# Optimization experiments

Hardware: AMD Instinct MI355X
Metric: run time of the kernel (lower is better)

Reference implementation:

```python
import jax, jax.numpy as jnp
import numpy as np

DIM = 768
HEADS = 12
HIDDEN = 3072  # int(dim * mlp_ratio)
DEGREE = 3
EPS = 1e-5


def layer_norm(x, g, b):
    m = jnp.mean(x, axis=-1, keepdims=True)
    v = jnp.mean((x - m) ** 2, axis=-1, keepdims=True)
    return (x - m) * jax.lax.rsqrt(v + EPS) * g + b


def cheby_layer(x, coeffs):
    # x: (B, N, I); coeffs: (I, O, DEGREE+1)
    t = jnp.tanh(x)
    theta = jnp.arccos(t)  # (B, N, I)
    d = jnp.arange(DEGREE + 1, dtype=x.dtype)
    basis = jnp.cos(theta[..., None] * d)  # (B, N, I, D)
    return jnp.einsum('bnid,iod->bno', basis, coeffs)


def setup_inputs() -> dict:
    key = jax.random.key(0)
    ks = jax.random.split(key, 9)
    B, N, C, H = 32, 197, DIM, HIDDEN
    x = jax.random.normal(ks[0], (B, N, C), dtype=jnp.float32)
    g1 = jnp.ones((C,), jnp.float32)
    b1 = jnp.zeros((C,), jnp.float32)
    w_qkv = jax.random.normal(ks[1], (C, 3 * C), jnp.float32) * (C ** -0.5)
    w_proj = jax.random.normal(ks[2], (C, C), jnp.float32) * (C ** -0.5)
    b_proj = jnp.zeros((C,), jnp.float32)
    g2 = jnp.ones((C,), jnp.float32)
    b2 = jnp.zeros((C,), jnp.float32)
    c1 = jax.random.normal(ks[3], (C, H, DEGREE + 1), jnp.float32) / (C * (DEGREE + 1))
    c2 = jax.random.normal(ks[4], (H, C, DEGREE + 1), jnp.float32) / (H * (DEGREE + 1))
    return {"x": x, "g1": g1, "b1": b1, "w_qkv": w_qkv, "w_proj": w_proj,
            "b_proj": b_proj, "g2": g2, "b2": b2, "c1": c1, "c2": c2}


def reference(x, g1, b1, w_qkv, w_proj, b_proj, g2, b2, c1, c2):
    B, N, C = x.shape
    hd = C // HEADS
    scale = hd ** -0.5
    # --- attention branch ---
    h = layer_norm(x, g1, b1)
    qkv = (h @ w_qkv).reshape(B, N, 3, HEADS, hd).transpose(2, 0, 3, 1, 4)
    q, k, v = qkv[0], qkv[1], qkv[2]  # (B, H, N, hd)
    attn = jax.nn.softmax(jnp.einsum('bhnd,bhmd->bhnm', q, k) * scale, axis=-1)
    o = jnp.einsum('bhnm,bhmd->bhnd', attn, v).transpose(0, 2, 1, 3).reshape(B, N, C)
    x = x + o @ w_proj + b_proj
    # --- ChebyKAN MLP branch ---
    h = layer_norm(x, g2, b2)
    h = cheby_layer(h, c1)   # (B, N, HIDDEN)
    h = cheby_layer(h, c2)   # (B, N, C)
    return x + h
```

## Files before the change

### kernel.cpp

```cpp
#include <hip/hip_runtime.h>
#include <hip/hip_bf16.h>
#include <cmath>
#include <cstdint>
#include <cstddef>

#define DEV __device__ __forceinline__

typedef __attribute__((ext_vector_type(4))) float f32x4;
typedef __attribute__((ext_vector_type(8))) short bf16x8;
typedef __attribute__((ext_vector_type(4))) unsigned int u32x4;
typedef __attribute__((ext_vector_type(4))) unsigned short u16x4;

constexpr int NBATCH = 32;
constexpr int SEQ    = 197;
constexpr int CH     = 768;
constexpr int H3     = 3 * CH;
constexpr int NHEADS = 12;
constexpr int HD     = 64;
constexpr int HID    = 3072;
constexpr int TOK    = NBATCH * SEQ;
constexpr int TOKP   = 6400;
constexpr int KSPLIT = 2;
constexpr float LNEPS = 1e-5f;

DEV unsigned short f2bf(float f) {
  unsigned int u = __builtin_bit_cast(unsigned int, f);
  u += 0x7fffu + ((u >> 16) & 1u);
  return (unsigned short)(u >> 16);
}
DEV float bf2f(unsigned short s) {
  unsigned int u = ((unsigned int)s) << 16;
  return __builtin_bit_cast(float, u);
}

DEV float fast_tanh(float x) {
  const float e = __expf(2.f * x);
  return 1.f - 2.f * __builtin_amdgcn_rcpf(e + 1.f);
}

DEV void async_copy16(void* lds, const void* gmem) {
  __builtin_amdgcn_global_load_lds(
      (const __attribute__((address_space(1))) unsigned int*)gmem,
      (__attribute__((address_space(3))) unsigned int*)lds, 16, 0, 0);
}

template <int DO_TANH>
__global__ void ln_kernel(const float* __restrict__ xin, const float* __restrict__ gg,
                          const float* __restrict__ bb, unsigned short* __restrict__ outp) {
  const int row  = blockIdx.x * 4 + (threadIdx.x >> 6);
  const int lane = threadIdx.x & 63;
  if (row >= TOK) {
    u16x4 z = {0, 0, 0, 0};
    #pragma unroll
    for (int c = 0; c < 3; ++c)
      *(u16x4*)&outp[(size_t)row * CH + c * 256 + lane * 4] = z;
    return;
  }
  f32x4 v[3];
  float s = 0.f, s2 = 0.f;
  #pragma unroll
  for (int c = 0; c < 3; ++c) {
    v[c] = *(const f32x4*)&xin[(size_t)row * CH + c * 256 + lane * 4];
    #pragma unroll
    for (int e = 0; e < 4; ++e) { s += v[c][e]; s2 += v[c][e] * v[c][e]; }
  }
  #pragma unroll
  for (int off = 32; off; off >>= 1) { s += __shfl_xor(s, off); s2 += __shfl_xor(s2, off); }
  const float mean = s * (1.f / CH);
  const float var  = s2 * (1.f / CH) - mean * mean;
  const float rs   = rsqrtf(var + LNEPS);
  #pragma unroll
  for (int c = 0; c < 3; ++c) {
    f32x4 gv = *(const f32x4*)&gg[c * 256 + lane * 4];
    f32x4 bv = *(const f32x4*)&bb[c * 256 + lane * 4];
    u16x4 o;
    #pragma unroll
    for (int e = 0; e < 4; ++e) {
      float f = (v[c][e] - mean) * rs * gv[e] + bv[e];
      if (DO_TANH) f = fast_tanh(f);
      o[e] = f2bf(f);
    }
    *(u16x4*)&outp[(size_t)row * CH + c * 256 + lane * 4] = o;
  }
}

__global__ void transpose_bf16(const float* __restrict__ in, unsigned short* __restrict__ outp,
                               int K, int N) {
  __shared__ unsigned short tile[64][65];
  const int k0 = blockIdx.x * 64, n0 = blockIdx.y * 64;
  const int tc = threadIdx.x & 63, tr = threadIdx.x >> 6;
  #pragma unroll
  for (int rr = 0; rr < 64; rr += 4)
    tile[rr + tr][tc] = f2bf(in[(size_t)(k0 + rr + tr) * N + n0 + tc]);
  __syncthreads();
  #pragma unroll
  for (int rr = 0; rr < 64; rr += 4)
    outp[(size_t)(n0 + rr + tr) * K + k0 + tc] = tile[tc][rr + tr];
}

__global__ void cheb_combine(const float* __restrict__ cc, unsigned short* __restrict__ outp,
                             float* __restrict__ partial, int I, int O) {
  __shared__ unsigned short t1[64][65];
  __shared__ unsigned short t2[64][65];
  __shared__ unsigned short t3[64][65];
  __shared__ float psum[4][64];
  const int i0 = blockIdx.x * 64, o0 = blockIdx.y * 64;
  const int tc = threadIdx.x & 63, tr = threadIdx.x >> 6;
  float bs = 0.f;
  #pragma unroll
  for (int rr = 0; rr < 64; rr += 4) {
    f32x4 v = *(const f32x4*)&cc[((size_t)(i0 + rr + tr) * O + (o0 + tc)) * 4];
    t1[rr + tr][tc] = f2bf(v[1] - 3.f * v[3]);
    t2[rr + tr][tc] = f2bf(2.f * v[2]);
    t3[rr + tr][tc] = f2bf(4.f * v[3]);
    bs += v[0] - v[2];
  }
  psum[tr][tc] = bs;
  __syncthreads();
  const size_t plane = (size_t)O * I;
  #pragma unroll
  for (int rr = 0; rr < 64; rr += 4) {
    size_t ob = (size_t)(o0 + rr + tr) * I + i0 + tc;
    outp[ob]             = t1[tc][rr + tr];
    outp[ob + plane]     = t2[tc][rr + tr];
    outp[ob + 2 * plane] = t3[tc][rr + tr];
  }
  if (tr == 0)
    partial[(size_t)blockIdx.x * O + o0 + tc] =
        psum[0][tc] + psum[1][tc] + psum[2][tc] + psum[3][tc];
}

__global__ void bias_finish(const float* __restrict__ partial, float* __restrict__ bias,
                            int nblk, int O) {
  const int o = blockIdx.x * 256 + threadIdx.x;
  float s = 0.f;
  for (int k = 0; k < nblk; ++k) s += partial[(size_t)k * O + o];
  bias[o] = s;
}

__global__ void zero_pad_rows(unsigned short* __restrict__ p) {
  const size_t idx = ((size_t)blockIdx.x * 256 + threadIdx.x) * 4;
  u16x4 z = {0, 0, 0, 0};
  *(u16x4*)&p[(size_t)TOK * CH + idx] = z;
}

template <int EPI>
__global__ __launch_bounds__(256)
void gemm_kernel(const unsigned short* __restrict__ A,
                 const unsigned short* __restrict__ BT,
                 const int Ktot, const int Nn,
                 const float* __restrict__ bias,
                 const float* __restrict__ resid,
                 void* __restrict__ Cout) {
  __shared__ __align__(16) unsigned short As[2][128 * 32];
  __shared__ __align__(16) unsigned short Bs[2][128 * 32];
  const int t = threadIdx.x;
  const int lane = t & 63;
  const int wid = t >> 6;
  const int wm = wid >> 1, wn = wid & 1;
  const int bm = blockIdx.x * 128;
  const int bn = blockIdx.y * 128;
  const int srow = t >> 2;
  const int scol = (t & 3) * 8;
  const int nkt = Ktot >> 5;
  f32x4 acc[4][4] = {};

  auto stage = [&](int buf, int kt) {
    const int kk = kt << 5;
    char* lb = (char*)&Bs[buf][0] + (wid << 10);
    async_copy16(lb,        &BT[(size_t)(bn + srow) * Ktot + kk + scol]);
    async_copy16(lb + 4096, &BT[(size_t)(bn + 64 + srow) * Ktot + kk + scol]);
    char* la = (char*)&As[buf][0] + (wid << 10);
    async_copy16(la,        &A[(size_t)(bm + srow) * Ktot + kk + scol]);
    async_copy16(la + 4096, &A[(size_t)(bm + 64 + srow) * Ktot + kk + scol]);
  };

  int cur = 0;
  stage(0, 0);
  for (int kt = 0; kt < nkt; ++kt) {
    if (kt + 1 < nkt) {
      stage(cur ^ 1, kt + 1);
      asm volatile("s_waitcnt vmcnt(4)" ::: "memory");
    } else {
      asm volatile("s_waitcnt vmcnt(0)" ::: "memory");
    }
    __builtin_amdgcn_s_barrier();
    __builtin_amdgcn_sched_barrier(0);
    bf16x8 af[4], bfr[4];
    const int frow = lane & 15;
    const int fk = (lane >> 4) * 8;
    #pragma unroll
    for (int m = 0; m < 4; ++m)
      af[m] = *(const bf16x8*)&As[cur][(wm * 64 + m * 16 + frow) * 32 + fk];
    #pragma unroll
    for (int n = 0; n < 4; ++n)
      bfr[n] = *(const bf16x8*)&Bs[cur][(wn * 64 + n * 16 + frow) * 32 + fk];
    #pragma unroll
    for (int m = 0; m < 4; ++m)
      #pragma unroll
      for (int n = 0; n < 4; ++n)
        acc[m][n] = __builtin_amdgcn_mfma_f32_16x16x32_bf16(af[m], bfr[n], acc[m][n], 0, 0, 0);
    __builtin_amdgcn_s_barrier();
    cur ^= 1;
  }
  #pragma unroll
  for (int m = 0; m < 4; ++m) {
    #pragma unroll
    for (int n = 0; n < 4; ++n) {
      #pragma unroll
      for (int r = 0; r < 4; ++r) {
        const int row = bm + wm * 64 + m * 16 + (lane >> 4) * 4 + r;
        const int col = bn + wn * 64 + n * 16 + (lane & 15);
        const float v = acc[m][n][r];
        if (EPI == 0) {
          ((unsigned short*)Cout)[(size_t)row * Nn + col] = f2bf(v);
        } else {
          float o = 0.f;
          if (row < TOK) o = v + bias[col] + resid[(size_t)row * Nn + col];
          ((float*)Cout)[(size_t)row * Nn + col] = o;
        }
      }
    }
  }
}

template <int EPI>
__global__ __launch_bounds__(256, 4)
void cheb_gemm(const unsigned short* __restrict__ A,
               const unsigned short* __restrict__ BT,
               const int Ktot, const int Nn, const int kchunk,
               const float* __restrict__ bias,
               void* __restrict__ Cout) {
  __shared__ __align__(16) unsigned short Bs[3][3 * 64 * 32];
  const int t = threadIdx.x, lane = t & 63, wid = t >> 6;
  const int bm = blockIdx.x * 128, bn = blockIdx.y * 64;
  const int kbase = (int)blockIdx.z * kchunk;
  const int nkt = kchunk >> 5;
  const int srow = t >> 2;
  const int ssw  = ((t & 3) ^ ((t >> 2) & 3) ^ ((t >> 4) & 3)) * 8;
  const int frow = lane & 15;
  const int rslot = ((lane >> 4) ^ (lane & 3) ^ ((lane >> 2) & 3)) * 8;
  const int arow = bm + wid * 32 + frow;
  const int ak   = (lane >> 4) * 8;
  const size_t pstride = (size_t)Nn * Ktot;
  f32x4 acc[2][4] = {};

  auto stageB = [&](int buf, int kt) {
    const int kk = kbase + (kt << 5);
    char* lb = (char*)&Bs[buf][0] + (wid << 10);
    #pragma unroll
    for (int p = 0; p < 3; ++p)
      async_copy16(lb + p * 4096,
                   &BT[(size_t)p * pstride + (size_t)(bn + srow) * Ktot + kk + ssw]);
  };
  auto loadA = [&](bf16x8 (&dst)[2], int kt) {
    const int kk = kbase + (kt << 5) + ak;
    #pragma unroll
    for (int m = 0; m < 2; ++m)
      dst[m] = *(const bf16x8*)&A[(size_t)(arow + m * 16) * Ktot + kk];
  };

  bf16x8 aA[2], aB[2];
  stageB(0, 0);
  loadA(aA, 0);
  if (nkt > 1) stageB(1, 1);

  auto body = [&](bf16x8 (&curA)[2], bf16x8 (&nxtA)[2], int kt) {
    if (kt + 1 < nkt) asm volatile("s_waitcnt vmcnt(3)" ::: "memory");
    else              asm volatile("s_waitcnt vmcnt(0)" ::: "memory");
    __builtin_amdgcn_s_barrier();
    __builtin_amdgcn_sched_barrier(0);
    const unsigned short* bp = &Bs[kt % 3][0];
    if (kt + 1 < nkt) loadA(nxtA, kt + 1);
    if (kt + 2 < nkt) stageB((kt + 2) % 3, kt + 2);
    bf16x8 a2[2], a3[2];
    #pragma unroll
    for (int m = 0; m < 2; ++m) {
      const unsigned int* w = (const unsigned int*)&curA[m];
      unsigned int sq[4], cu[4];
      #pragma unroll
      for (int j = 0; j < 4; ++j) {
        const unsigned int u = w[j];
        const float lo = __builtin_bit_cast(float, u << 16);
        const float hi = __builtin_bit_cast(float, u & 0xffff0000u);
        const float lo2 = lo * lo, hi2 = hi * hi;
        const float lo3 = lo2 * lo, hi3 = hi2 * hi;
        sq[j] = (__builtin_bit_cast(unsigned int, hi2) & 0xffff0000u) |
                (__builtin_bit_cast(unsigned int, lo2) >> 16);
        cu[j] = (__builtin_bit_cast(unsigned int, hi3) & 0xffff0000u) |
                (__builtin_bit_cast(unsigned int, lo3) >> 16);
      }
      a2[m] = *(const bf16x8*)sq;
      a3[m] = *(const bf16x8*)cu;
    }
    #pragma unroll
    for (int p = 0; p < 3; ++p) {
      bf16x8 br[4];
      #pragma unroll
      for (int n = 0; n < 4; ++n)
        br[n] = *(const bf16x8*)&bp[(p * 64 + n * 16 + frow) * 32 + rslot];
      #pragma unroll
      for (int m = 0; m < 2; ++m) {
        const bf16x8 a = (p == 0) ? curA[m] : (p == 1) ? a2[m] : a3[m];
        #pragma unroll
        for (int n = 0; n < 4; ++n)
          acc[m][n] = __builtin_amdgcn_mfma_f32_16x16x32_bf16(a, br[n], acc[m][n], 0, 0, 0);
      }
    }
  };

  for (int kt = 0; kt < nkt; kt += 2) {
    body(aA, aB, kt);
    body(aB, aA, kt + 1);
  }

  #pragma unroll
  for (int m = 0; m < 2; ++m) {
    #pragma unroll
    for (int n = 0; n < 4; ++n) {
      #pragma unroll
      for (int r = 0; r < 4; ++r) {
        const int row = bm + wid * 32 + m * 16 + (lane >> 4) * 4 + r;
        const int col = bn + n * 16 + (lane & 15);
        const float v = acc[m][n][r];
        if (EPI == 0) {
          ((unsigned short*)Cout)[(size_t)row * Nn + col] = f2bf(fast_tanh(v + bias[col]));
        } else {
          ((float*)Cout)[((size_t)blockIdx.z * TOKP + row) * Nn + col] = v;
        }
      }
    }
  }
}

__global__ void cheb2_reduce(const float* __restrict__ part, const float* __restrict__ bias,
                             const float* __restrict__ resid, float* __restrict__ outp) {
  const size_t idx = ((size_t)blockIdx.x * 256 + threadIdx.x) * 4;
  const int col = (int)(idx % CH);
  f32x4 s = *(const f32x4*)&part[idx];
  #pragma unroll
  for (int z = 1; z < KSPLIT; ++z) {
    f32x4 p = *(const f32x4*)&part[(size_t)z * TOKP * CH + idx];
    #pragma unroll
    for (int e = 0; e < 4; ++e) s[e] += p[e];
  }
  const f32x4 bv = *(const f32x4*)&bias[col];
  const f32x4 rv = *(const f32x4*)&resid[idx];
  f32x4 o;
  #pragma unroll
  for (int e = 0; e < 4; ++e) o[e] = s[e] + bv[e] + rv[e];
  *(f32x4*)&outp[idx] = o;
}

__global__ __launch_bounds__(256)
void attn_kernel(const unsigned short* __restrict__ qkv, unsigned short* __restrict__ aout) {
  constexpr int VSTR = 232;
  __shared__ __align__(16) unsigned short Vlds[64 * VSTR];
  __shared__ __align__(16) unsigned short Plds[4][16 * VSTR];
  const int bh = blockIdx.x;
  const int b = bh / NHEADS, hh = bh - b * NHEADS;
  const int t = threadIdx.x, lane = t & 63, wid = t >> 6;
  const size_t base = (size_t)b * SEQ * H3;
  const int part = t & 7, key0 = t >> 3;
  for (int it = 0; it < 7; ++it) {
    const int key = key0 + it * 32;
    u32x4 raw = {0, 0, 0, 0};
    if (key < SEQ)
      raw = *(const u32x4*)&qkv[base + (size_t)key * H3 + 2 * CH + hh * HD + part * 8];
    const unsigned short* us = (const unsigned short*)&raw;
    #pragma unroll
    for (int e = 0; e < 8; ++e)
      Vlds[(part * 8 + e) * VSTR + key] = us[e];
  }
  for (int idx = t; idx < 4 * 16 * 16; idx += 256) {
    const int buf = idx >> 8, rr = (idx >> 4) & 15, ccc = idx & 15;
    Plds[buf][rr * VSTR + 208 + ccc] = 0;
  }
  __syncthreads();

  for (int qt = wid; qt < 13; qt += 4) {
    const int qrow = qt * 16 + (lane & 15);
    const size_t qbase = base + (size_t)qrow * H3 + hh * HD + (lane >> 4) * 8;
    const bf16x8 qf0 = *(const bf16x8*)&qkv[qbase];
    const bf16x8 qf1 = *(const bf16x8*)&qkv[qbase + 32];
    float sv[13][4];
    #pragma unroll
    for (int ktile = 0; ktile < 13; ++ktile) {
      const int keyc = ktile * 16 + (lane & 15);
      const size_t kbase = base + (size_t)keyc * H3 + CH + hh * HD + (lane >> 4) * 8;
      const bf16x8 kf0 = *(const bf16x8*)&qkv[kbase];
      const bf16x8 kf1 = *(const bf16x8*)&qkv[kbase + 32];
      f32x4 s = {0.f, 0.f, 0.f, 0.f};
      s = __builtin_amdgcn_mfma_f32_16x16x32_bf16(qf0, kf0, s, 0, 0, 0);
      s = __builtin_amdgcn_mfma_f32_16x16x32_bf16(qf1, kf1, s, 0, 0, 0);
      const bool valid = keyc < SEQ;
      #pragma unroll
      for (int r = 0; r < 4; ++r)
        sv[ktile][r] = valid ? s[r] * 0.125f : -INFINITY;
    }
    float rsum[4];
    #pragma unroll
    for (int r = 0; r < 4; ++r) {
      float mx = -INFINITY;
      #pragma unroll
      for (int kt2 = 0; kt2 < 13; ++kt2) mx = fmaxf(mx, sv[kt2][r]);
      #pragma unroll
      for (int off = 1; off < 16; off <<= 1) mx = fmaxf(mx, __shfl_xor(mx, off));
      float sum = 0.f;
      #pragma unroll
      for (int kt2 = 0; kt2 < 13; ++kt2) {
        const float p = __expf(sv[kt2][r] - mx);
        sv[kt2][r] = p;
        sum += p;
      }
      #pragma unroll
      for (int off = 1; off < 16; off <<= 1) sum += __shfl_xor(sum, off);
      rsum[r] = sum;
    }
    const int g4 = (lane >> 4) * 4;
    #pragma unroll
    for (int kt2 = 0; kt2 < 13; ++kt2)
      #pragma unroll
      for (int r = 0; r < 4; ++r)
        Plds[wid][(g4 + r) * VSTR + kt2 * 16 + (lane & 15)] = f2bf(sv[kt2][r]);
    asm volatile("s_waitcnt lgkmcnt(0)" ::: "memory");
    f32x4 oacc[4] = {};
    #pragma unroll
    for (int ks = 0; ks < 7; ++ks) {
      const bf16x8 pf = *(const bf16x8*)&Plds[wid][(lane & 15) * VSTR + ks * 32 + (lane >> 4) * 8];
      #pragma unroll
      for (int n = 0; n < 4; ++n) {
        const bf16x8 vf = *(const bf16x8*)&Vlds[(n * 16 + (lane & 15)) * VSTR + ks * 32 + (lane >> 4) * 8];
        oacc[n] = __builtin_amdgcn_mfma_f32_16x16x32_bf16(pf, vf, oacc[n], 0, 0, 0);
      }
    }
    #pragma unroll
    for (int n = 0; n < 4; ++n)
      #pragma unroll
      for (int r = 0; r < 4; ++r) {
        const int q = qt * 16 + g4 + r;
        if (q < SEQ) {
          const float val = oacc[n][r] / rsum[r];
          aout[(size_t)(b * SEQ + q) * CH + hh * HD + n * 16 + (lane & 15)] = f2bf(val);
        }
      }
  }
}

extern "C" void kernel_launch(void* const* d_in, const int* in_sizes, int n_in,
                              void* d_out, int out_size, void* d_ws, size_t ws_size,
                              hipStream_t stream) {
  const float* x      = (const float*)d_in[0];
  const float* g1     = (const float*)d_in[1];
  const float* b1     = (const float*)d_in[2];
  const float* w_qkv  = (const float*)d_in[3];
  const float* w_proj = (const float*)d_in[4];
  const float* b_proj = (const float*)d_in[5];
  const float* g2     = (const float*)d_in[6];
  const float* b2     = (const float*)d_in[7];
  const float* c1     = (const float*)d_in[8];
  const float* c2     = (const float*)d_in[9];

  char* ws = (char*)d_ws;
  size_t off = 0;
  auto alloc = [&](size_t bytes) { size_t o = off; off += (bytes + 255) & ~(size_t)255; return o; };
  unsigned short* h      = (unsigned short*)(ws + alloc((size_t)TOKP * CH * 2));
  unsigned short* wqkvT  = (unsigned short*)(ws + alloc((size_t)H3 * CH * 2));
  unsigned short* wprojT = (unsigned short*)(ws + alloc((size_t)CH * CH * 2));
  unsigned short* c1T    = (unsigned short*)(ws + alloc((size_t)3 * HID * CH * 2));
  unsigned short* c2T    = (unsigned short*)(ws + alloc((size_t)3 * CH * HID * 2));
  float* bias1           = (float*)(ws + alloc((size_t)HID * 4));
  float* bias2           = (float*)(ws + alloc((size_t)CH * 4));
  float* part1           = (float*)(ws + alloc((size_t)(CH / 64) * HID * 4));
  float* part2           = (float*)(ws + alloc((size_t)(HID / 64) * CH * 4));
  unsigned short* qkvb   = (unsigned short*)(ws + alloc((size_t)TOKP * H3 * 2));
  unsigned short* aoutb  = (unsigned short*)(ws + alloc((size_t)TOKP * CH * 2));
  float* xmid            = (float*)(ws + alloc((size_t)TOKP * CH * 4));
  unsigned short* tb     = (unsigned short*)(ws + alloc((size_t)TOKP * CH * 2));
  unsigned short* ub     = (unsigned short*)(ws + alloc((size_t)TOKP * HID * 2));
  float* partK           = (float*)(ws + alloc((size_t)KSPLIT * TOKP * CH * 4));
  (void)ws_size; (void)in_sizes; (void)n_in; (void)out_size;

  transpose_bf16<<<dim3(CH / 64, H3 / 64), 256, 0, stream>>>(w_qkv, wqkvT, CH, H3);
  transpose_bf16<<<dim3(CH / 64, CH / 64), 256, 0, stream>>>(w_proj, wprojT, CH, CH);
  cheb_combine<<<dim3(CH / 64, HID / 64), 256, 0, stream>>>(c1, c1T, part1, CH, HID);
  cheb_combine<<<dim3(HID / 64, CH / 64), 256, 0, stream>>>(c2, c2T, part2, HID, CH);
  bias_finish<<<dim3(HID / 256), 256, 0, stream>>>(part1, bias1, CH / 64, HID);
  bias_finish<<<dim3(CH / 256), 256, 0, stream>>>(part2, bias2, HID / 64, CH);
  zero_pad_rows<<<dim3(72), 256, 0, stream>>>(aoutb);

  ln_kernel<0><<<dim3(TOKP / 4), 256, 0, stream>>>(x, g1, b1, h);
  gemm_kernel<0><<<dim3(TOKP / 128, H3 / 128), 256, 0, stream>>>(h, wqkvT, CH, H3,
                                                                 nullptr, nullptr, qkvb);
  attn_kernel<<<dim3(NBATCH * NHEADS), 256, 0, stream>>>(qkvb, aoutb);
  gemm_kernel<1><<<dim3(TOKP / 128, CH / 128), 256, 0, stream>>>(aoutb, wprojT, CH, CH,
                                                                 b_proj, x, xmid);
  ln_kernel<1><<<dim3(TOKP / 4), 256, 0, stream>>>(xmid, g2, b2, tb);
  cheb_gemm<0><<<dim3(TOKP / 128, HID / 64, 1), 256, 0, stream>>>(tb, c1T, CH, HID, CH,
                                                                  bias1, ub);
  cheb_gemm<1><<<dim3(TOKP / 128, CH / 64, KSPLIT), 256, 0, stream>>>(ub, c2T, HID, CH,
                                                                      HID / KSPLIT,
                                                                      nullptr, partK);
  cheb2_reduce<<<dim3(TOK * CH / 1024), 256, 0, stream>>>(partK, bias2, xmid, (float*)d_out);
}
```

Before: 427.1 us.

## Drop split-K for second Chebyshev GEMM and split attention query tiles across two blocks

The second Chebyshev GEMM now runs without split-K and applies bias plus residual directly in its epilogue. This removes the partial-sum buffer and the separate reduce kernel, at the cost of a grid half as large (600 blocks) with twice the K-loop length. Separately, the attention kernel is launched with a second grid dimension, so each block handles half of the query tiles. That doubles the number of attention blocks, but each block still reloads V into LDS, so that staging work is duplicated.

```diff
diff --git a/kernel.cpp b/kernel.cpp
--- a/kernel.cpp
+++ b/kernel.cpp
@@ -20,7 +20,6 @@
 constexpr int HID    = 3072;
 constexpr int TOK    = NBATCH * SEQ;
 constexpr int TOKP   = 6400;
-constexpr int KSPLIT = 2;
 constexpr float LNEPS = 1e-5f;
 
 DEV unsigned short f2bf(float f) {
@@ -230,6 +229,7 @@
                const unsigned short* __restrict__ BT,
                const int Ktot, const int Nn, const int kchunk,
                const float* __restrict__ bias,
+               const float* __restrict__ resid,
                void* __restrict__ Cout) {
   __shared__ __align__(16) unsigned short Bs[3][3 * 64 * 32];
   const int t = threadIdx.x, lane = t & 63, wid = t >> 6;
@@ -326,30 +326,12 @@
         if (EPI == 0) {
           ((unsigned short*)Cout)[(size_t)row * Nn + col] = f2bf(fast_tanh(v + bias[col]));
         } else {
-          ((float*)Cout)[((size_t)blockIdx.z * TOKP + row) * Nn + col] = v;
+          if (row < TOK)
+            ((float*)Cout)[(size_t)row * Nn + col] = v + bias[col] + resid[(size_t)row * Nn + col];
         }
       }
     }
   }
-}
-
-__global__ void cheb2_reduce(const float* __restrict__ part, const float* __restrict__ bias,
-                             const float* __restrict__ resid, float* __restrict__ outp) {
-  const size_t idx = ((size_t)blockIdx.x * 256 + threadIdx.x) * 4;
-  const int col = (int)(idx % CH);
-  f32x4 s = *(const f32x4*)&part[idx];
-  #pragma unroll
-  for (int z = 1; z < KSPLIT; ++z) {
-    f32x4 p = *(const f32x4*)&part[(size_t)z * TOKP * CH + idx];
-    #pragma unroll
-    for (int e = 0; e < 4; ++e) s[e] += p[e];
-  }
-  const f32x4 bv = *(const f32x4*)&bias[col];
-  const f32x4 rv = *(const f32x4*)&resid[idx];
-  f32x4 o;
-  #pragma unroll
-  for (int e = 0; e < 4; ++e) o[e] = s[e] + bv[e] + rv[e];
-  *(f32x4*)&outp[idx] = o;
 }
 
 __global__ __launch_bounds__(256)
@@ -358,6 +340,7 @@
   __shared__ __align__(16) unsigned short Vlds[64 * VSTR];
   __shared__ __align__(16) unsigned short Plds[4][16 * VSTR];
   const int bh = blockIdx.x;
+  const int by = blockIdx.y;
   const int b = bh / NHEADS, hh = bh - b * NHEADS;
   const int t = threadIdx.x, lane = t & 63, wid = t >> 6;
   const size_t base = (size_t)b * SEQ * H3;
@@ -378,7 +361,7 @@
   }
   __syncthreads();
 
-  for (int qt = wid; qt < 13; qt += 4) {
+  for (int qt = wid + 4 * by; qt < 13; qt += 8) {
     const int qrow = qt * 16 + (lane & 15);
     const size_t qbase = base + (size_t)qrow * H3 + hh * HD + (lane >> 4) * 8;
     const bf16x8 qf0 = *(const bf16x8*)&qkv[qbase];
@@ -478,7 +461,6 @@
   float* xmid            = (float*)(ws + alloc((size_t)TOKP * CH * 4));
   unsigned short* tb     = (unsigned short*)(ws + alloc((size_t)TOKP * CH * 2));
   unsigned short* ub     = (unsigned short*)(ws + alloc((size_t)TOKP * HID * 2));
-  float* partK           = (float*)(ws + alloc((size_t)KSPLIT * TOKP * CH * 4));
   (void)ws_size; (void)in_sizes; (void)n_in; (void)out_size;
 
   transpose_bf16<<<dim3(CH / 64, H3 / 64), 256, 0, stream>>>(w_qkv, wqkvT, CH, H3);
@@ -492,14 +474,12 @@
   ln_kernel<0><<<dim3(TOKP / 4), 256, 0, stream>>>(x, g1, b1, h);
   gemm_kernel<0><<<dim3(TOKP / 128, H3 / 128), 256, 0, stream>>>(h, wqkvT, CH, H3,
                                                                  nullptr, nullptr, qkvb);
-  attn_kernel<<<dim3(NBATCH * NHEADS), 256, 0, stream>>>(qkvb, aoutb);
+  attn_kernel<<<dim3(NBATCH * NHEADS, 2), 256, 0, stream>>>(qkvb, aoutb);
   gemm_kernel<1><<<dim3(TOKP / 128, CH / 128), 256, 0, stream>>>(aoutb, wprojT, CH, CH,
                                                                  b_proj, x, xmid);
   ln_kernel<1><<<dim3(TOKP / 4), 256, 0, stream>>>(xmid, g2, b2, tb);
   cheb_gemm<0><<<dim3(TOKP / 128, HID / 64, 1), 256, 0, stream>>>(tb, c1T, CH, HID, CH,
-                                                                  bias1, ub);
-  cheb_gemm<1><<<dim3(TOKP / 128, CH / 64, KSPLIT), 256, 0, stream>>>(ub, c2T, HID, CH,
-                                                                      HID / KSPLIT,
-                                                                      nullptr, partK);
-  cheb2_reduce<<<dim3(TOK * CH / 1024), 256, 0, stream>>>(partK, bias2, xmid, (float*)d_out);
-}
+                                                                  bias1, nullptr, ub);
+  cheb_gemm<1><<<dim3(TOKP / 128, CH / 64, 1), 256, 0, stream>>>(ub, c2T, HID, CH, HID,
+                                                                 bias2, xmid, (float*)d_out);
+}
```

After: 434.7 us. No clear change (+1.8%).
